# Optimization experiments

Measured on AMD Instinct MI355X. Metric: run time of the kernel, lower is better.

Reference implementation:

```python
import jax, jax.numpy as jnp
import numpy as np

B, S = 2, 2048
H = 16
NOPE, ROPE, VD = 128, 64, 128
Q_RANK, KV_RANK = 1536, 512
SCALE = 1.0 / np.sqrt(NOPE + ROPE)  # 1/sqrt(192)
NEG_INF = -10000.0


def _make_rope(n_pos, dim):
    # matches gen_rope: theta over even indices, angles repeated twice (rotate-half layout)
    theta = 1.0 / (10000.0 ** (np.arange(0, dim, 2, dtype=np.float32) / dim))
    pos = np.arange(n_pos, dtype=np.float32)
    ang = np.outer(pos, theta)                      # [N, dim/2]
    ang = np.concatenate([ang, ang], axis=-1)       # [N, dim]
    return jnp.asarray(np.cos(ang)), jnp.asarray(np.sin(ang))


def _rope(x, cos, sin):
    # rotate-half RoPE; cos/sin broadcast over head dim if present
    d = x.shape[-1]
    x1, x2 = x[..., : d // 2], x[..., d // 2 :]
    rot = jnp.concatenate([-x2, x1], axis=-1)
    return x * cos + rot * sin


def setup_inputs() -> dict:
    key = jax.random.key(0)
    ks = jax.random.split(key, 5)
    Q = jax.random.normal(ks[0], (B, S, Q_RANK), dtype=jnp.float32)
    KV = jax.random.normal(ks[1], (B, S, KV_RANK), dtype=jnp.float32)
    PE = jax.random.normal(ks[2], (B, S, ROPE), dtype=jnp.float32)
    WUQ = jax.random.normal(ks[3], (H * (NOPE + ROPE), Q_RANK), dtype=jnp.float32) * 0.02
    WUKV = jax.random.normal(ks[4], (H * (NOPE + VD), KV_RANK), dtype=jnp.float32) * 0.02
    cos, sin = _make_rope(B * S, ROPE)
    cos = cos.reshape(B, S, ROPE)
    sin = sin.reshape(B, S, ROPE)
    mask = jnp.triu(jnp.full((S, S), NEG_INF, dtype=jnp.float32), k=1)
    return {"Q": Q, "KV": KV, "PE": PE, "WUQ": WUQ, "WUKV": WUKV,
            "cos": cos, "sin": sin, "mask": mask}


def reference(Q, KV, PE, WUQ, WUKV, cos, sin, mask):
    b, s, _ = Q.shape
    # low-rank up-projections
    q = jnp.einsum("bsl,dl->bsd", Q, WUQ).reshape(b, s, H, NOPE + ROPE)
    q_nope, q_pe = q[..., :NOPE], q[..., NOPE:]
    q_pe = _rope(q_pe, cos[:, :, None, :], sin[:, :, None, :])

    kv = jnp.einsum("bsl,dl->bsd", KV, WUKV).reshape(b, s, H, NOPE + VD)
    k_nope, v = kv[..., :NOPE], kv[..., NOPE:]
    k_pe = _rope(PE, cos, sin)  # [b, s, ROPE], shared across heads

    # attention scores: per-head nope part + shared rope part
    scores = jnp.einsum("bqhd,bkhd->bhqk", q_nope, k_nope)
    scores = scores + jnp.einsum("bqhd,bkd->bhqk", q_pe, k_pe)
    scores = scores * SCALE + mask[None, None, :, :]
    attn = jax.nn.softmax(scores, axis=-1)
    out = jnp.einsum("bhqk,bkhd->bqhd", attn, v)  # [b, s, H, VD]
    return out
```

## Files before the change

### kernel.cpp

```cpp
#include <hip/hip_runtime.h>

typedef __attribute__((ext_vector_type(8))) short short8;
typedef __attribute__((ext_vector_type(4))) float f32x4;

#define SS 2048
#define HH 16
#define NOPE_D 128
#define ROPE_D 64
#define VDIM 128
#define QD 192
#define SCALE_F 0.07216878364870323f
#define LOG2E 1.4426950408889634f

__device__ __forceinline__ unsigned short f2bf(float f) {
    unsigned int x = __builtin_bit_cast(unsigned int, f);
    unsigned int r = (x + 0x7fffu + ((x >> 16) & 1u)) >> 16;
    return (unsigned short)r;
}

#define GLDS16(g, l) __builtin_amdgcn_global_load_lds( \
    (const __attribute__((address_space(1))) void*)(g), \
    (__attribute__((address_space(3))) void*)(l), 16, 0, 0)

__global__ __launch_bounds__(256) void cvt_all(
    const float* __restrict__ Q, const float* __restrict__ WUQ,
    const float* __restrict__ KV, const float* __restrict__ WUKV,
    const float* __restrict__ PE, const float* __restrict__ cs, const float* __restrict__ sn,
    unsigned short* __restrict__ Qb, unsigned short* __restrict__ WUQb,
    unsigned short* __restrict__ KVb, unsigned short* __restrict__ WUKVb,
    unsigned short* __restrict__ kpe)
{
    int bid = blockIdx.x;
    if (bid >= 14848) {
        int idx = (bid - 14848) * 256 + threadIdx.x;
        int i = idx & 31, row = idx >> 5;
        float x1 = PE[row * 64 + i], x2 = PE[row * 64 + 32 + i];
        float c1 = cs[row * 64 + i],      s1 = sn[row * 64 + i];
        float c2 = cs[row * 64 + 32 + i], s2 = sn[row * 64 + 32 + i];
        kpe[row * 64 + i]      = f2bf(x1 * c1 - x2 * s1);
        kpe[row * 64 + 32 + i] = f2bf(x2 * c2 + x1 * s2);
        return;
    }
    const float* src; unsigned short* dst; float scale = 1.0f;
    if (bid < 6144)       { src = Q;    dst = Qb; }
    else if (bid < 10752) { src = WUQ;  dst = WUQb; bid -= 6144; scale = SCALE_F * LOG2E; }
    else if (bid < 12800) { src = KV;   dst = KVb;  bid -= 10752; }
    else                  { src = WUKV; dst = WUKVb; bid -= 12800; }
    int i = (bid * 256 + threadIdx.x) * 4;
    float4 v = *(const float4*)(src + i);
    ushort4 o = { f2bf(v.x * scale), f2bf(v.y * scale), f2bf(v.z * scale), f2bf(v.w * scale) };
    *(ushort4*)(dst + i) = o;
}

__global__ __launch_bounds__(256) void gemm_fused(
    const unsigned short* __restrict__ Qb, const unsigned short* __restrict__ WUQb,
    const unsigned short* __restrict__ KVb, const unsigned short* __restrict__ WUKVb,
    unsigned short* __restrict__ qbuf, unsigned short* __restrict__ knope,
    unsigned short* __restrict__ vT,
    const float* __restrict__ cs, const float* __restrict__ sn)
{
    __shared__ unsigned short As[128 * 64];
    __shared__ unsigned short Bs[128 * 64];
    const int t = threadIdx.x, w = t >> 6, lane = t & 63;
    const int n16 = lane & 15, quad = lane >> 4;

    int bid = blockIdx.x;
    const unsigned short *A, *B; int N, K, bm, bn; bool g1;
    if (bid < 768) { g1 = true;  A = Qb;  B = WUQb;  N = 3072; K = 1536;
                     bm = (bid / 24) * 128; bn = (bid % 24) * 128; }
    else           { g1 = false; bid -= 768; A = KVb; B = WUKVb; N = 4096; K = 512;
                     bm = (bid / 32) * 128; bn = (bid % 32) * 128; }

    const int wm = (w >> 1) * 64, wn = (w & 1) * 64;
    f32x4 acc[4][4] = {};

    const int lr = lane >> 3, lc = lane & 7;
    const int sw = (lc ^ lr) * 8;
    const unsigned short* gA = A + (size_t)(bm + w * 32 + lr) * K + sw;
    const unsigned short* gB = B + (size_t)(bn + w * 32 + lr) * K + sw;

    for (int k0 = 0; k0 < K; k0 += 64) {
        __syncthreads();
        for (int j = 0; j < 4; j++) {
            GLDS16(gA + (size_t)j * 8 * K + k0, &As[(w * 32 + j * 8) * 64]);
            GLDS16(gB + (size_t)j * 8 * K + k0, &Bs[(w * 32 + j * 8) * 64]);
        }
        __syncthreads();
        for (int ks = 0; ks < 2; ks++) {
            short8 af[4], bf[4];
            for (int mt = 0; mt < 4; mt++) {
                int rw = wm + mt * 16 + n16;
                af[mt] = *(const short8*)&As[rw * 64 + (((ks * 4 + quad) ^ (rw & 7)) * 8)];
            }
            for (int nt = 0; nt < 4; nt++) {
                int rw = wn + nt * 16 + n16;
                bf[nt] = *(const short8*)&Bs[rw * 64 + (((ks * 4 + quad) ^ (rw & 7)) * 8)];
            }
            for (int mt = 0; mt < 4; mt++)
                for (int nt = 0; nt < 4; nt++)
                    acc[mt][nt] = __builtin_amdgcn_mfma_f32_16x16x32_bf16(af[mt], bf[nt], acc[mt][nt], 0, 0, 0);
        }
    }

    const int colbase = bn + wn;
    if (g1) {
        const bool is_pe = ((colbase % 192) >= 128);
        if (is_pe) {
            for (int mt = 0; mt < 4; mt++)
                for (int r = 0; r < 4; r++) {
                    int row = bm + wm + mt * 16 + quad * 4 + r;
                    const float* cr = cs + row * 64;
                    const float* sr = sn + row * 64;
                    for (int nt = 0; nt < 2; nt++) {
                        int i = nt * 16 + n16;
                        float x1 = acc[mt][nt][r], x2 = acc[mt][nt + 2][r];
                        float o1 = x1 * cr[i] - x2 * sr[i];
                        float o2 = x2 * cr[32 + i] + x1 * sr[32 + i];
                        qbuf[(size_t)row * N + colbase + i] = f2bf(o1);
                        qbuf[(size_t)row * N + colbase + 32 + i] = f2bf(o2);
                    }
                }
        } else {
            for (int mt = 0; mt < 4; mt++)
                for (int nt = 0; nt < 4; nt++)
                    for (int r = 0; r < 4; r++)
                        qbuf[(size_t)(bm + wm + mt * 16 + quad * 4 + r) * N + colbase + nt * 16 + n16]
                            = f2bf(acc[mt][nt][r]);
        }
    } else {
        if ((colbase & 255) < 128) {
            for (int mt = 0; mt < 4; mt++)
                for (int nt = 0; nt < 4; nt++) {
                    int col = colbase + nt * 16 + n16;
                    int h = col >> 8, d = col & 255;
                    for (int r = 0; r < 4; r++)
                        knope[(size_t)(bm + wm + mt * 16 + quad * 4 + r) * 2048 + h * 128 + d]
                            = f2bf(acc[mt][nt][r]);
                }
        } else {
            for (int mt = 0; mt < 4; mt++)
                for (int nt = 0; nt < 4; nt++) {
                    int col = colbase + nt * 16 + n16;
                    int h = col >> 8, vd = (col & 255) - 128;
                    int row0 = bm + wm + mt * 16 + quad * 4;
                    int b = row0 >> 11, s0 = row0 & 2047;
                    int l6 = s0 & 63;
                    int scol = (s0 & ~63) + ((l6 >> 5) & 1) * 32 + ((l6 >> 2) & 3) * 8
                             + ((l6 >> 4) & 1) * 4 + (l6 & 3);
                    ushort4 pk = { f2bf(acc[mt][nt][0]), f2bf(acc[mt][nt][1]),
                                   f2bf(acc[mt][nt][2]), f2bf(acc[mt][nt][3]) };
                    *(ushort4*)&vT[((size_t)(b * 16 + h) * 128 + vd) * 2048 + scol] = pk;
                }
        }
    }
}

__global__ __launch_bounds__(256, 2) void attn_kernel(
    const unsigned short* __restrict__ qbuf,
    const unsigned short* __restrict__ knope,
    const unsigned short* __restrict__ kpe,
    const unsigned short* __restrict__ vT,
    float* __restrict__ out,
    int* __restrict__ qc)
{
    const int t = threadIdx.x, w = t >> 6, lane = t & 63;
    const int n16 = lane & 15, quad = lane >> 4;

    __shared__ unsigned short Kn[64 * 128];
    __shared__ unsigned short Kp[64 * 64];
    __shared__ unsigned short Vt[128 * 64];
    __shared__ float Al[4][32];
    __shared__ int su;

    while (true) {
        __syncthreads();
        if (t == 0) su = atomicAdd(qc, 1);
        __syncthreads();
        const int u = su;
        if (u >= 512) break;
        const int qt = 15 - (u >> 5);
        const int c = u & 31;
        const int h = c & 15, b = c >> 4;

        const unsigned short* knb = knope + (size_t)b * 2048 * 2048 + h * 128;
        const unsigned short* kpb = kpe + (size_t)b * 2048 * 64;
        const unsigned short* vtb = vT + (size_t)(b * 16 + h) * 128 * 2048;

        short8 qf[2][6];
        for (int qg = 0; qg < 2; qg++) {
            size_t grow = (size_t)(b * SS + qt * 128 + w * 32 + qg * 16 + n16);
            const unsigned short* qp = qbuf + grow * (HH * QD) + h * QD + quad * 8;
            for (int ks = 0; ks < 6; ks++) qf[qg][ks] = *(const short8*)(qp + ks * 32);
        }

        f32x4 O[2][8] = {};
        float m_i[2] = { -INFINITY, -INFINITY };
        float l_i[2] = { 0.f, 0.f };

        const int nkt = 2 * qt + 2;
        for (int kt = 0; kt < nkt; kt++) {
            __syncthreads();
            {
                int r = w * 16 + (lane >> 4);
                int sl = lane & 15;
                for (int j = 0; j < 4; j++) {
                    int rr = r + j * 4;
                    const unsigned short* g = knb + (size_t)(kt * 64 + rr) * 2048 + ((sl ^ (rr & 7)) * 8);
                    GLDS16(g, &Kn[(w * 16 + j * 4) * 128]);
                }
            }
            {
                int r = w * 16 + (lane >> 3);
                int sl = lane & 7;
                for (int j = 0; j < 2; j++) {
                    int rr = r + j * 8;
                    const unsigned short* g = kpb + (size_t)(kt * 64 + rr) * 64 + ((sl ^ (rr & 7)) * 8);
                    GLDS16(g, &Kp[(w * 16 + j * 8) * 64]);
                }
            }
            {
                int r = w * 32 + (lane >> 3);
                int sl = lane & 7;
                for (int j = 0; j < 4; j++) {
                    int rr = r + j * 8;
                    const unsigned short* g = vtb + (size_t)rr * 2048 + kt * 64 + ((sl ^ (rr & 7)) * 8);
                    GLDS16(g, &Vt[(w * 32 + j * 8) * 64]);
                }
            }
            __syncthreads();

            f32x4 Sg[2][4];
            for (int nt = 0; nt < 4; nt++) {
                int key = nt * 16 + n16, kx = key & 7;
                f32x4 a0 = {}, a1 = {};
                for (int ks = 0; ks < 4; ks++) {
                    short8 af = *(const short8*)&Kn[key * 128 + (((ks * 4 + quad) ^ kx) * 8)];
                    a0 = __builtin_amdgcn_mfma_f32_16x16x32_bf16(af, qf[0][ks], a0, 0, 0, 0);
                    a1 = __builtin_amdgcn_mfma_f32_16x16x32_bf16(af, qf[1][ks], a1, 0, 0, 0);
                }
                for (int ks = 0; ks < 2; ks++) {
                    short8 af = *(const short8*)&Kp[key * 64 + (((ks * 4 + quad) ^ kx) * 8)];
                    a0 = __builtin_amdgcn_mfma_f32_16x16x32_bf16(af, qf[0][4 + ks], a0, 0, 0, 0);
                    a1 = __builtin_amdgcn_mfma_f32_16x16x32_bf16(af, qf[1][4 + ks], a1, 0, 0, 0);
                }
                Sg[0][nt] = a0; Sg[1][nt] = a1;
            }

            if (kt >= 2 * qt) {
                for (int qg = 0; qg < 2; qg++) {
                    int qq = qt * 128 + w * 32 + qg * 16 + n16;
                    for (int nt = 0; nt < 4; nt++) {
                        int key0 = kt * 64 + nt * 16 + quad * 4;
                        for (int r = 0; r < 4; r++)
                            if (key0 + r > qq) Sg[qg][nt][r] = -INFINITY;
                    }
                }
            }

            float alpha[2];
            for (int qg = 0; qg < 2; qg++) {
                float mx = -INFINITY;
                for (int nt = 0; nt < 4; nt++)
                    for (int r = 0; r < 4; r++) mx = fmaxf(mx, Sg[qg][nt][r]);
                mx = fmaxf(mx, __shfl_xor(mx, 16, 64));
                mx = fmaxf(mx, __shfl_xor(mx, 32, 64));
                float mnew = fmaxf(m_i[qg], mx);
                alpha[qg] = exp2f(m_i[qg] - mnew);
                m_i[qg] = mnew;
                float rs = 0.f;
                for (int nt = 0; nt < 4; nt++)
                    for (int r = 0; r < 4; r++) {
                        float pv = exp2f(Sg[qg][nt][r] - mnew);
                        Sg[qg][nt][r] = pv;
                        rs += pv;
                    }
                l_i[qg] = l_i[qg] * alpha[qg] + rs;
            }
            if (quad == 0) { Al[w][n16] = alpha[0]; Al[w][16 + n16] = alpha[1]; }
            f32x4 av0 = *(const f32x4*)&Al[w][quad * 4];
            f32x4 av1 = *(const f32x4*)&Al[w][16 + quad * 4];
            for (int v8 = 0; v8 < 8; v8++)
                for (int r = 0; r < 4; r++) {
                    O[0][v8][r] *= av0[r];
                    O[1][v8][r] *= av1[r];
                }

            short8 pp[2][2];
            for (int qg = 0; qg < 2; qg++)
                for (int ntp = 0; ntp < 2; ntp++) {
                    short8 pa;
                    for (int j = 0; j < 4; j++) pa[j] = (short)f2bf(Sg[qg][ntp * 2][j]);
                    for (int j = 0; j < 4; j++) pa[4 + j] = (short)f2bf(Sg[qg][ntp * 2 + 1][j]);
                    pp[qg][ntp] = pa;
                }
            for (int ntp = 0; ntp < 2; ntp++)
                for (int v8 = 0; v8 < 8; v8++) {
                    int vd = v8 * 16 + n16;
                    short8 vb = *(const short8*)&Vt[vd * 64 + (((ntp * 4 + quad) ^ (vd & 7)) * 8)];
                    O[0][v8] = __builtin_amdgcn_mfma_f32_16x16x32_bf16(pp[0][ntp], vb, O[0][v8], 0, 0, 0);
                    O[1][v8] = __builtin_amdgcn_mfma_f32_16x16x32_bf16(pp[1][ntp], vb, O[1][v8], 0, 0, 0);
                }
        }

        {
            float l0 = l_i[0];
            l0 += __shfl_xor(l0, 16, 64); l0 += __shfl_xor(l0, 32, 64);
            float l1 = l_i[1];
            l1 += __shfl_xor(l1, 16, 64); l1 += __shfl_xor(l1, 32, 64);
            if (quad == 0) { Al[w][n16] = 1.f / l0; Al[w][16 + n16] = 1.f / l1; }
        }
        f32x4 lv0 = *(const f32x4*)&Al[w][quad * 4];
        f32x4 lv1 = *(const f32x4*)&Al[w][16 + quad * 4];
        for (int qg = 0; qg < 2; qg++) {
            const f32x4 lv = qg ? lv1 : lv0;
            for (int r = 0; r < 4; r++) {
                size_t qrow = (size_t)(b * SS + qt * 128 + w * 32 + qg * 16 + quad * 4 + r);
                float* op = out + (qrow * HH + h) * VDIM;
                for (int v8 = 0; v8 < 8; v8++)
                    op[v8 * 16 + n16] = O[qg][v8][r] * lv[r];
            }
        }
    }
}

extern "C" void kernel_launch(void* const* d_in, const int* in_sizes, int n_in,
                              void* d_out, int out_size, void* d_ws, size_t ws_size,
                              hipStream_t stream) {
    const float* Q    = (const float*)d_in[0];
    const float* KV   = (const float*)d_in[1];
    const float* PE   = (const float*)d_in[2];
    const float* WUQ  = (const float*)d_in[3];
    const float* WUKV = (const float*)d_in[4];
    const float* cosp = (const float*)d_in[5];
    const float* sinp = (const float*)d_in[6];
    float* out = (float*)d_out;

    unsigned short* qbuf  = (unsigned short*)d_ws;
    unsigned short* knope = qbuf  + (size_t)4096 * 3072;
    unsigned short* vT    = knope + (size_t)4096 * 2048;
    unsigned short* kpe   = vT    + (size_t)4096 * 2048;
    unsigned short* Qb    = kpe   + (size_t)4096 * 64;
    unsigned short* WUQb  = Qb    + (size_t)4096 * 1536;
    unsigned short* KVb   = WUQb  + (size_t)3072 * 1536;
    unsigned short* WUKVb = KVb   + (size_t)4096 * 512;
    int* qcounter = (int*)(WUKVb + (size_t)4096 * 512);

    hipMemsetAsync(qcounter, 0, 4, stream);
    cvt_all<<<15360, 256, 0, stream>>>(Q, WUQ, KV, WUKV, PE, cosp, sinp,
                                       Qb, WUQb, KVb, WUKVb, kpe);
    gemm_fused<<<1792, 256, 0, stream>>>(Qb, WUQb, KVb, WUKVb,
                                         qbuf, knope, vT, cosp, sinp);
    attn_kernel<<<512, 256, 0, stream>>>(qbuf, knope, kpe, vT, out, qcounter);
}
```

Measured before the change: 302.4 us.

## Double-buffer K/V tiles in attention, load k_pe to registers, static block scheduling

The attention kernel now double-buffers the K-nope and V^T shared-memory tiles, so global-to-LDS loads for the next key tile overlap compute on the current one, with one barrier per tile instead of two. The shared k_pe rope keys are read straight from global memory into registers rather than staged through LDS. The atomic work-queue loop is replaced by a static blockIdx mapping that pairs long and short causal tiles across the grid, which also drops the memset and atomic. LDS use roughly doubles, which could limit occupancy, and the static mapping gives up dynamic load balancing.

```diff
diff --git a/kernel.cpp b/kernel.cpp
--- a/kernel.cpp
+++ b/kernel.cpp
@@ -155,170 +155,165 @@
     }
 }
 
+#define STAGE(bufsel, kt_) do { \
+    int r_ = w * 16 + (lane >> 4), sl_ = lane & 15; \
+    for (int j = 0; j < 4; j++) { \
+        int rr_ = r_ + j * 4; \
+        GLDS16(knb + (size_t)((kt_) * 64 + rr_) * 2048 + ((sl_ ^ (rr_ & 7)) * 8), \
+               &Kn[bufsel][(w * 16 + j * 4) * 128]); \
+    } \
+    int r2_ = w * 32 + (lane >> 3), sl2_ = lane & 7; \
+    for (int j = 0; j < 4; j++) { \
+        int rr_ = r2_ + j * 8; \
+        GLDS16(vtb + (size_t)rr_ * 2048 + (kt_) * 64 + ((sl2_ ^ (rr_ & 7)) * 8), \
+               &Vt[bufsel][(w * 32 + j * 8) * 64]); \
+    } \
+} while (0)
+
+#define LOADKP(kp_, kt_) do { \
+    const unsigned short* kpt_ = kpb + (size_t)((kt_) * 64) * 64; \
+    for (int nt = 0; nt < 4; nt++) \
+        for (int ks = 0; ks < 2; ks++) \
+            kp_[nt * 2 + ks] = *(const short8*)(kpt_ + (nt * 16 + n16) * 64 + (ks * 4 + quad) * 8); \
+} while (0)
+
+#define COMPUTE(KnB, VtB, kp_, kt_) do { \
+    f32x4 Sg[2][4]; \
+    for (int nt = 0; nt < 4; nt++) { \
+        int key = nt * 16 + n16, kx = key & 7; \
+        f32x4 a0 = {}, a1 = {}; \
+        for (int ks = 0; ks < 4; ks++) { \
+            short8 af = *(const short8*)&(KnB)[key * 128 + (((ks * 4 + quad) ^ kx) * 8)]; \
+            a0 = __builtin_amdgcn_mfma_f32_16x16x32_bf16(af, qf[0][ks], a0, 0, 0, 0); \
+            a1 = __builtin_amdgcn_mfma_f32_16x16x32_bf16(af, qf[1][ks], a1, 0, 0, 0); \
+        } \
+        for (int ks = 0; ks < 2; ks++) { \
+            a0 = __builtin_amdgcn_mfma_f32_16x16x32_bf16(kp_[nt * 2 + ks], qf[0][4 + ks], a0, 0, 0, 0); \
+            a1 = __builtin_amdgcn_mfma_f32_16x16x32_bf16(kp_[nt * 2 + ks], qf[1][4 + ks], a1, 0, 0, 0); \
+        } \
+        Sg[0][nt] = a0; Sg[1][nt] = a1; \
+    } \
+    if ((kt_) >= 2 * qt) {    \
+        for (int qg = 0; qg < 2; qg++) { \
+            int qq = qt * 128 + w * 32 + qg * 16 + n16; \
+            for (int nt = 0; nt < 4; nt++) { \
+                int key0 = (kt_) * 64 + nt * 16 + quad * 4; \
+                for (int r = 0; r < 4; r++) \
+                    if (key0 + r > qq) Sg[qg][nt][r] = -INFINITY; \
+            } \
+        } \
+    } \
+     \
+    float alpha[2]; \
+    for (int qg = 0; qg < 2; qg++) { \
+        float mx = -INFINITY; \
+        for (int nt = 0; nt < 4; nt++) \
+            for (int r = 0; r < 4; r++) mx = fmaxf(mx, Sg[qg][nt][r]); \
+        mx = fmaxf(mx, __shfl_xor(mx, 16, 64)); \
+        mx = fmaxf(mx, __shfl_xor(mx, 32, 64)); \
+        float mnew = fmaxf(m_i[qg], mx); \
+        alpha[qg] = exp2f(m_i[qg] - mnew); \
+        m_i[qg] = mnew; \
+        float rs = 0.f; \
+        for (int nt = 0; nt < 4; nt++) \
+            for (int r = 0; r < 4; r++) { \
+                float pv = exp2f(Sg[qg][nt][r] - mnew); \
+                Sg[qg][nt][r] = pv; \
+                rs += pv; \
+            } \
+        l_i[qg] = l_i[qg] * alpha[qg] + rs; \
+    } \
+    if (quad == 0) { Al[w][n16] = alpha[0]; Al[w][16 + n16] = alpha[1]; } \
+    f32x4 av0 = *(const f32x4*)&Al[w][quad * 4]; \
+    f32x4 av1 = *(const f32x4*)&Al[w][16 + quad * 4]; \
+    for (int v8 = 0; v8 < 8; v8++) \
+        for (int r = 0; r < 4; r++) { \
+            O[0][v8][r] *= av0[r]; \
+            O[1][v8][r] *= av1[r]; \
+        } \
+     \
+    short8 pp[2][2]; \
+    for (int qg = 0; qg < 2; qg++) \
+        for (int ntp = 0; ntp < 2; ntp++) { \
+            short8 pa; \
+            for (int j = 0; j < 4; j++) pa[j] = (short)f2bf(Sg[qg][ntp * 2][j]); \
+            for (int j = 0; j < 4; j++) pa[4 + j] = (short)f2bf(Sg[qg][ntp * 2 + 1][j]); \
+            pp[qg][ntp] = pa; \
+        } \
+    for (int ntp = 0; ntp < 2; ntp++) \
+        for (int v8 = 0; v8 < 8; v8++) { \
+            int vd = v8 * 16 + n16; \
+            short8 vb = *(const short8*)&(VtB)[vd * 64 + (((ntp * 4 + quad) ^ (vd & 7)) * 8)]; \
+            O[0][v8] = __builtin_amdgcn_mfma_f32_16x16x32_bf16(pp[0][ntp], vb, O[0][v8], 0, 0, 0); \
+            O[1][v8] = __builtin_amdgcn_mfma_f32_16x16x32_bf16(pp[1][ntp], vb, O[1][v8], 0, 0, 0); \
+        } \
+} while (0)
+
 __global__ __launch_bounds__(256, 2) void attn_kernel(
     const unsigned short* __restrict__ qbuf,
     const unsigned short* __restrict__ knope,
     const unsigned short* __restrict__ kpe,
     const unsigned short* __restrict__ vT,
-    float* __restrict__ out,
-    int* __restrict__ qc)
+    float* __restrict__ out)
 {
     const int t = threadIdx.x, w = t >> 6, lane = t & 63;
     const int n16 = lane & 15, quad = lane >> 4;
 
-    __shared__ unsigned short Kn[64 * 128];
-    __shared__ unsigned short Kp[64 * 64];
-    __shared__ unsigned short Vt[128 * 64];
+    __shared__ unsigned short Kn[2][64 * 128];
+    __shared__ unsigned short Vt[2][128 * 64];
     __shared__ float Al[4][32];
-    __shared__ int su;
-
-    while (true) {
+
+    const int u = blockIdx.x;
+    int qt, c;
+    if (u < 256) { qt = 15 - (u >> 5); c = u & 31; }
+    else         { qt = (u - 256) >> 5; c = u & 31; }
+    const int h = c & 15, b = c >> 4;
+
+    const unsigned short* knb = knope + (size_t)b * 2048 * 2048 + h * 128;
+    const unsigned short* kpb = kpe + (size_t)b * 2048 * 64;
+    const unsigned short* vtb = vT + (size_t)(b * 16 + h) * 128 * 2048;
+
+    short8 qf[2][6];
+    for (int qg = 0; qg < 2; qg++) {
+        size_t grow = (size_t)(b * SS + qt * 128 + w * 32 + qg * 16 + n16);
+        const unsigned short* qp = qbuf + grow * (HH * QD) + h * QD + quad * 8;
+        for (int ks = 0; ks < 6; ks++) qf[qg][ks] = *(const short8*)(qp + ks * 32);
+    }
+
+    f32x4 O[2][8] = {};
+    float m_i[2] = { -INFINITY, -INFINITY };
+    float l_i[2] = { 0.f, 0.f };
+    short8 kpA[8], kpB[8];
+
+    const int nkt = 2 * qt + 2;
+
+    STAGE(0, 0); LOADKP(kpA, 0);
+    __syncthreads();
+    for (int kt2 = 0; kt2 < nkt; kt2 += 2) {
+        STAGE(1, kt2 + 1); LOADKP(kpB, kt2 + 1);
+        COMPUTE(Kn[0], Vt[0], kpA, kt2);
         __syncthreads();
-        if (t == 0) su = atomicAdd(qc, 1);
+        if (kt2 + 2 < nkt) { STAGE(0, kt2 + 2); LOADKP(kpA, kt2 + 2); }
+        COMPUTE(Kn[1], Vt[1], kpB, kt2 + 1);
         __syncthreads();
-        const int u = su;
-        if (u >= 512) break;
-        const int qt = 15 - (u >> 5);
-        const int c = u & 31;
-        const int h = c & 15, b = c >> 4;
-
-        const unsigned short* knb = knope + (size_t)b * 2048 * 2048 + h * 128;
-        const unsigned short* kpb = kpe + (size_t)b * 2048 * 64;
-        const unsigned short* vtb = vT + (size_t)(b * 16 + h) * 128 * 2048;
-
-        short8 qf[2][6];
-        for (int qg = 0; qg < 2; qg++) {
-            size_t grow = (size_t)(b * SS + qt * 128 + w * 32 + qg * 16 + n16);
-            const unsigned short* qp = qbuf + grow * (HH * QD) + h * QD + quad * 8;
-            for (int ks = 0; ks < 6; ks++) qf[qg][ks] = *(const short8*)(qp + ks * 32);
-        }
-
-        f32x4 O[2][8] = {};
-        float m_i[2] = { -INFINITY, -INFINITY };
-        float l_i[2] = { 0.f, 0.f };
-
-        const int nkt = 2 * qt + 2;
-        for (int kt = 0; kt < nkt; kt++) {
-            __syncthreads();
-            {
-                int r = w * 16 + (lane >> 4);
-                int sl = lane & 15;
-                for (int j = 0; j < 4; j++) {
-                    int rr = r + j * 4;
-                    const unsigned short* g = knb + (size_t)(kt * 64 + rr) * 2048 + ((sl ^ (rr & 7)) * 8);
-                    GLDS16(g, &Kn[(w * 16 + j * 4) * 128]);
-                }
-            }
-            {
-                int r = w * 16 + (lane >> 3);
-                int sl = lane & 7;
-                for (int j = 0; j < 2; j++) {
-                    int rr = r + j * 8;
-                    const unsigned short* g = kpb + (size_t)(kt * 64 + rr) * 64 + ((sl ^ (rr & 7)) * 8);
-                    GLDS16(g, &Kp[(w * 16 + j * 8) * 64]);
-                }
-            }
-            {
-                int r = w * 32 + (lane >> 3);
-                int sl = lane & 7;
-                for (int j = 0; j < 4; j++) {
-                    int rr = r + j * 8;
-                    const unsigned short* g = vtb + (size_t)rr * 2048 + kt * 64 + ((sl ^ (rr & 7)) * 8);
-                    GLDS16(g, &Vt[(w * 32 + j * 8) * 64]);
-                }
-            }
-            __syncthreads();
-
-            f32x4 Sg[2][4];
-            for (int nt = 0; nt < 4; nt++) {
-                int key = nt * 16 + n16, kx = key & 7;
-                f32x4 a0 = {}, a1 = {};
-                for (int ks = 0; ks < 4; ks++) {
-                    short8 af = *(const short8*)&Kn[key * 128 + (((ks * 4 + quad) ^ kx) * 8)];
-                    a0 = __builtin_amdgcn_mfma_f32_16x16x32_bf16(af, qf[0][ks], a0, 0, 0, 0);
-                    a1 = __builtin_amdgcn_mfma_f32_16x16x32_bf16(af, qf[1][ks], a1, 0, 0, 0);
-                }
-                for (int ks = 0; ks < 2; ks++) {
-                    short8 af = *(const short8*)&Kp[key * 64 + (((ks * 4 + quad) ^ kx) * 8)];
-                    a0 = __builtin_amdgcn_mfma_f32_16x16x32_bf16(af, qf[0][4 + ks], a0, 0, 0, 0);
-                    a1 = __builtin_amdgcn_mfma_f32_16x16x32_bf16(af, qf[1][4 + ks], a1, 0, 0, 0);
-                }
-                Sg[0][nt] = a0; Sg[1][nt] = a1;
-            }
-
-            if (kt >= 2 * qt) {
-                for (int qg = 0; qg < 2; qg++) {
-                    int qq = qt * 128 + w * 32 + qg * 16 + n16;
-                    for (int nt = 0; nt < 4; nt++) {
-                        int key0 = kt * 64 + nt * 16 + quad * 4;
-                        for (int r = 0; r < 4; r++)
-                            if (key0 + r > qq) Sg[qg][nt][r] = -INFINITY;
-                    }
-                }
-            }
-
-            float alpha[2];
-            for (int qg = 0; qg < 2; qg++) {
-                float mx = -INFINITY;
-                for (int nt = 0; nt < 4; nt++)
-                    for (int r = 0; r < 4; r++) mx = fmaxf(mx, Sg[qg][nt][r]);
-                mx = fmaxf(mx, __shfl_xor(mx, 16, 64));
-                mx = fmaxf(mx, __shfl_xor(mx, 32, 64));
-                float mnew = fmaxf(m_i[qg], mx);
-                alpha[qg] = exp2f(m_i[qg] - mnew);
-                m_i[qg] = mnew;
-                float rs = 0.f;
-                for (int nt = 0; nt < 4; nt++)
-                    for (int r = 0; r < 4; r++) {
-                        float pv = exp2f(Sg[qg][nt][r] - mnew);
-                        Sg[qg][nt][r] = pv;
-                        rs += pv;
-                    }
-                l_i[qg] = l_i[qg] * alpha[qg] + rs;
-            }
-            if (quad == 0) { Al[w][n16] = alpha[0]; Al[w][16 + n16] = alpha[1]; }
-            f32x4 av0 = *(const f32x4*)&Al[w][quad * 4];
-            f32x4 av1 = *(const f32x4*)&Al[w][16 + quad * 4];
+    }
+
+    {
+        float l0 = l_i[0];
+        l0 += __shfl_xor(l0, 16, 64); l0 += __shfl_xor(l0, 32, 64);
+        float l1 = l_i[1];
+        l1 += __shfl_xor(l1, 16, 64); l1 += __shfl_xor(l1, 32, 64);
+        if (quad == 0) { Al[w][n16] = 1.f / l0; Al[w][16 + n16] = 1.f / l1; }
+    }
+    f32x4 lv0 = *(const f32x4*)&Al[w][quad * 4];
+    f32x4 lv1 = *(const f32x4*)&Al[w][16 + quad * 4];
+    for (int qg = 0; qg < 2; qg++) {
+        const f32x4 lv = qg ? lv1 : lv0;
+        for (int r = 0; r < 4; r++) {
+            size_t qrow = (size_t)(b * SS + qt * 128 + w * 32 + qg * 16 + quad * 4 + r);
+            float* op = out + (qrow * HH + h) * VDIM;
             for (int v8 = 0; v8 < 8; v8++)
-                for (int r = 0; r < 4; r++) {
-                    O[0][v8][r] *= av0[r];
-                    O[1][v8][r] *= av1[r];
-                }
-
-            short8 pp[2][2];
-            for (int qg = 0; qg < 2; qg++)
-                for (int ntp = 0; ntp < 2; ntp++) {
-                    short8 pa;
-                    for (int j = 0; j < 4; j++) pa[j] = (short)f2bf(Sg[qg][ntp * 2][j]);
-                    for (int j = 0; j < 4; j++) pa[4 + j] = (short)f2bf(Sg[qg][ntp * 2 + 1][j]);
-                    pp[qg][ntp] = pa;
-                }
-            for (int ntp = 0; ntp < 2; ntp++)
-                for (int v8 = 0; v8 < 8; v8++) {
-                    int vd = v8 * 16 + n16;
-                    short8 vb = *(const short8*)&Vt[vd * 64 + (((ntp * 4 + quad) ^ (vd & 7)) * 8)];
-                    O[0][v8] = __builtin_amdgcn_mfma_f32_16x16x32_bf16(pp[0][ntp], vb, O[0][v8], 0, 0, 0);
-                    O[1][v8] = __builtin_amdgcn_mfma_f32_16x16x32_bf16(pp[1][ntp], vb, O[1][v8], 0, 0, 0);
-                }
-        }
-
-        {
-            float l0 = l_i[0];
-            l0 += __shfl_xor(l0, 16, 64); l0 += __shfl_xor(l0, 32, 64);
-            float l1 = l_i[1];
-            l1 += __shfl_xor(l1, 16, 64); l1 += __shfl_xor(l1, 32, 64);
-            if (quad == 0) { Al[w][n16] = 1.f / l0; Al[w][16 + n16] = 1.f / l1; }
-        }
-        f32x4 lv0 = *(const f32x4*)&Al[w][quad * 4];
-        f32x4 lv1 = *(const f32x4*)&Al[w][16 + quad * 4];
-        for (int qg = 0; qg < 2; qg++) {
-            const f32x4 lv = qg ? lv1 : lv0;
-            for (int r = 0; r < 4; r++) {
-                size_t qrow = (size_t)(b * SS + qt * 128 + w * 32 + qg * 16 + quad * 4 + r);
-                float* op = out + (qrow * HH + h) * VDIM;
-                for (int v8 = 0; v8 < 8; v8++)
-                    op[v8 * 16 + n16] = O[qg][v8][r] * lv[r];
-            }
+                op[v8 * 16 + n16] = O[qg][v8][r] * lv[r];
         }
     }
 }
@@ -343,12 +338,10 @@
     unsigned short* WUQb  = Qb    + (size_t)4096 * 1536;
     unsigned short* KVb   = WUQb  + (size_t)3072 * 1536;
     unsigned short* WUKVb = KVb   + (size_t)4096 * 512;
-    int* qcounter = (int*)(WUKVb + (size_t)4096 * 512);
-
-    hipMemsetAsync(qcounter, 0, 4, stream);
+
     cvt_all<<<15360, 256, 0, stream>>>(Q, WUQ, KV, WUKV, PE, cosp, sinp,
                                        Qb, WUQb, KVb, WUKVb, kpe);
     gemm_fused<<<1792, 256, 0, stream>>>(Qb, WUQb, KVb, WUKVb,
                                          qbuf, knope, vT, cosp, sinp);
-    attn_kernel<<<512, 256, 0, stream>>>(qbuf, knope, kpe, vT, out, qcounter);
-}
+    attn_kernel<<<512, 256, 0, stream>>>(qbuf, knope, kpe, vT, out);
+}
```

Result: slower. 414.4 us (+37.1%).
